# Kernel optimization log

Measured on AMD Instinct MI355X. Metric: run time of the kernel, lower is better.

The kernel has to match this reference:

```python
import jax, jax.numpy as jnp
import numpy as np

M_BUCKETS = 2048  # input_features // q = 4096 // 2


def countsketch(x, hash_idx, rand_sgn, m=M_BUCKETS):
    # x: [N, D]; scatter-add signed columns into m buckets -> [N, m]
    return jnp.zeros((x.shape[0], m), x.dtype).at[:, hash_idx].add(x * rand_sgn[None, :])


def setup_inputs() -> dict:
    key = jax.random.key(0)
    k1, k2, k3, k4, k5 = jax.random.split(key, 5)
    B, D, O = 4096, 4096, 4096
    inp = jax.random.normal(k1, (B, D), dtype=jnp.float32)
    # match torch init: weight uniform(-sqrt(3)/sqrt(D), sqrt(3)/sqrt(D)), bias uniform(-1/sqrt(D), 1/sqrt(D))
    bound = 1.0 / np.sqrt(D)
    weight = jax.random.uniform(k2, (O, D), dtype=jnp.float32,
                                minval=-bound * np.sqrt(3.0), maxval=bound * np.sqrt(3.0))
    bias = jax.random.uniform(k3, (O,), dtype=jnp.float32, minval=-bound, maxval=bound)
    hash_idx = jax.random.randint(k4, (D,), 0, M_BUCKETS, dtype=jnp.int32)
    rand_sgn = (2.0 * jax.random.randint(k5, (D,), 0, 2).astype(jnp.float32) - 1.0)
    return {"input": inp, "weight": weight, "bias": bias,
            "hash_idx": hash_idx, "rand_sgn": rand_sgn}


def reference(input, weight, bias, hash_idx, rand_sgn):
    input_sketch = countsketch(input, hash_idx, rand_sgn)    # [B, m]
    weight_sketch = countsketch(weight, hash_idx, rand_sgn)  # [O, m]
    out = input_sketch @ weight_sketch.T + bias[None, :]     # [B, O]
    return out
```

## Files before the change

kernel.cpp:

```cpp
#include <hip/hip_runtime.h>
#include <hip/hip_bf16.h>
#include <stdint.h>

#define D_DIM     4096
#define MB        2048
#define NROWS     4096
#define K_DIM     MB

typedef __bf16 bf16x8 __attribute__((ext_vector_type(8)));
typedef float  floatx4 __attribute__((ext_vector_type(4)));

__device__ __forceinline__ void gld_lds16(const void* g, void* l) {
    __builtin_amdgcn_global_load_lds(
        (const __attribute__((address_space(1))) unsigned int*)g,
        (__attribute__((address_space(3))) unsigned int*)l,
        16, 0, 0);
}

__global__ __launch_bounds__(256) void build_csr(
    const int* __restrict__ hash_idx,
    unsigned int* __restrict__ desc,
    unsigned short* __restrict__ perm16)
{
    __shared__ int cnt[MB];
    __shared__ int scan[MB];
    const int t = threadIdx.x;

    for (int k = t; k < MB; k += 256) cnt[k] = 0;
    __syncthreads();
    for (int j = t; j < D_DIM; j += 256) atomicAdd(&cnt[hash_idx[j]], 1);
    __syncthreads();
    for (int k = t; k < MB; k += 256) scan[k] = cnt[k];
    __syncthreads();
    for (int stride = 1; stride < MB; stride <<= 1) {
        int vals[8];
        #pragma unroll
        for (int i = 0; i < 8; ++i) {
            int k = t + 256 * i;
            vals[i] = (k >= stride) ? scan[k - stride] : 0;
        }
        __syncthreads();
        #pragma unroll
        for (int i = 0; i < 8; ++i) scan[t + 256 * i] += vals[i];
        __syncthreads();
    }
    for (int k = t; k < MB; k += 256) {
        int excl = scan[k] - cnt[k];
        desc[k] = ((unsigned)excl << 16) | (unsigned)cnt[k];
        cnt[k] = excl;
    }
    __syncthreads();
    for (int j = t; j < D_DIM; j += 256) {
        int k = hash_idx[j];
        int pos = atomicAdd(&cnt[k], 1);
        perm16[pos] = (unsigned short)j;
    }
}

__global__ __launch_bounds__(256) void sketch_gather(
    const float* __restrict__ input,
    const float* __restrict__ weight,
    const float* __restrict__ rand_sgn,
    const unsigned int* __restrict__ desc,
    const unsigned short* __restrict__ perm16,
    __hip_bfloat16* __restrict__ sk_in,
    __hip_bfloat16* __restrict__ sk_w)
{
    __shared__ __align__(16) float rv0[D_DIM + 8];
    __shared__ __align__(16) float rv1[D_DIM + 8];
    __shared__ __align__(16) unsigned short perm[D_DIM];
    const int b = blockIdx.x;
    const bool is_w = (b >= NROWS / 2);
    const int pr = is_w ? (b - NROWS / 2) : b;
    const float* src = (is_w ? weight : input) + (size_t)pr * 2 * D_DIM;
    __hip_bfloat16* dst = (is_w ? sk_w : sk_in) + (size_t)pr * 2 * MB;
    const int t = threadIdx.x;

    const uint4* pg = (const uint4*)perm16;
    ((uint4*)perm)[t]       = pg[t];
    ((uint4*)perm)[t + 256] = pg[t + 256];

    const float4* s4 = (const float4*)src;
    const float4* g4 = (const float4*)rand_sgn;
    #pragma unroll
    for (int i = 0; i < 4; ++i) {
        int q = t + 256 * i;
        float4 g = g4[q];
        float4 x0 = s4[q], x1 = s4[q + 1024];
        float4 y0; y0.x = x0.x*g.x; y0.y = x0.y*g.y; y0.z = x0.z*g.z; y0.w = x0.w*g.w;
        float4 y1; y1.x = x1.x*g.x; y1.y = x1.y*g.y; y1.z = x1.z*g.z; y1.w = x1.w*g.w;
        *(float4*)&rv0[4 * q] = y0;
        *(float4*)&rv1[4 * q] = y1;
    }
    __syncthreads();

    float4 a0[4], a1[4];
    #pragma unroll
    for (int i = 0; i < 4; ++i) {
        int q = t + 256 * i;
        ushort4 pp = *(const ushort4*)&perm[4 * q];
        a0[i].x = rv0[pp.x]; a0[i].y = rv0[pp.y];
        a0[i].z = rv0[pp.z]; a0[i].w = rv0[pp.w];
        a1[i].x = rv1[pp.x]; a1[i].y = rv1[pp.y];
        a1[i].z = rv1[pp.z]; a1[i].w = rv1[pp.w];
    }
    __syncthreads();
    #pragma unroll
    for (int i = 0; i < 4; ++i) {
        int q = t + 256 * i;
        *(float4*)&rv0[4 * q] = a0[i];
        *(float4*)&rv1[4 * q] = a1[i];
    }
    __syncthreads();

    #pragma unroll
    for (int i = 0; i < 8; ++i) {
        int k = t + 256 * i;
        unsigned d = desc[k];
        int st = (int)(d >> 16), c = (int)(d & 0xFFFF);
        float s0 = 0.f, s1 = 0.f;
        #pragma unroll
        for (int j = 0; j < 8; ++j) {
            float v0 = rv0[st + j], v1 = rv1[st + j];
            bool m = (j < c);
            s0 += m ? v0 : 0.f;
            s1 += m ? v1 : 0.f;
        }
        for (int j = 8; j < c; ++j) {
            s0 += rv0[st + j]; s1 += rv1[st + j];
        }
        dst[k]      = __float2bfloat16(s0);
        dst[MB + k] = __float2bfloat16(s1);
    }
}

__global__ __launch_bounds__(256) void gemm_bt_bias(
    const __hip_bfloat16* __restrict__ A,
    const __hip_bfloat16* __restrict__ B,
    const float* __restrict__ bias,
    float* __restrict__ C)
{
    __shared__ __align__(16) __hip_bfloat16 lA[128 * 64];
    __shared__ __align__(16) __hip_bfloat16 lB[128 * 64];

    const int t = threadIdx.x;
    const int lane = t & 63;
    const int wid  = t >> 6;
    const int warpM = wid & 1, warpN = wid >> 1;
    const int quad = lane >> 4;
    const int mrow = lane & 15;
    const int rowBase = blockIdx.y * 128;
    const int colBase = blockIdx.x * 128;

    const __hip_bfloat16* gA[4];
    const __hip_bfloat16* gB[4];
    #pragma unroll
    for (int p = 0; p < 4; ++p) {
        int G = t + 256 * p;
        int m = G >> 3;
        int q = (G & 7) ^ (m & 7);
        gA[p] = A + (size_t)(rowBase + m) * K_DIM + q * 8;
        gB[p] = B + (size_t)(colBase + m) * K_DIM + q * 8;
    }
    __hip_bfloat16* sA = &lA[t * 8];
    __hip_bfloat16* sB = &lB[t * 8];

    floatx4 acc[4][4];
    const floatx4 zero = {0.f, 0.f, 0.f, 0.f};
    #pragma unroll
    for (int i = 0; i < 4; ++i)
        #pragma unroll
        for (int j = 0; j < 4; ++j) acc[i][j] = zero;

    for (int kb = 0; kb < K_DIM; kb += 64) {
        #pragma unroll
        for (int p = 0; p < 4; ++p) {
            gld_lds16(gA[p] + kb, sA + p * 2048);
            gld_lds16(gB[p] + kb, sB + p * 2048);
        }
        __syncthreads();

        #pragma unroll
        for (int h = 0; h < 2; ++h) {
            bf16x8 af[4], bfr[4];
            #pragma unroll
            for (int i = 0; i < 4; ++i) {
                int mA = warpM * 64 + i * 16 + mrow;
                int sa = (h * 4 + quad) ^ (mA & 7);
                af[i] = *(const bf16x8*)&lA[(mA * 8 + sa) * 8];
                int mB = warpN * 64 + i * 16 + mrow;
                int sb = (h * 4 + quad) ^ (mB & 7);
                bfr[i] = *(const bf16x8*)&lB[(mB * 8 + sb) * 8];
            }
            #pragma unroll
            for (int i = 0; i < 4; ++i)
                #pragma unroll
                for (int j = 0; j < 4; ++j)
                    acc[i][j] = __builtin_amdgcn_mfma_f32_16x16x32_bf16(
                        af[i], bfr[j], acc[i][j], 0, 0, 0);
        }
        __syncthreads();
    }

    float bj[4];
    #pragma unroll
    for (int j = 0; j < 4; ++j) bj[j] = bias[colBase + warpN * 64 + j * 16 + mrow];
    #pragma unroll
    for (int i = 0; i < 4; ++i) {
        int m0 = rowBase + warpM * 64 + i * 16 + quad * 4;
        #pragma unroll
        for (int j = 0; j < 4; ++j) {
            int n = colBase + warpN * 64 + j * 16 + mrow;
            #pragma unroll
            for (int p = 0; p < 4; ++p)
                C[(size_t)(m0 + p) * NROWS + n] = acc[i][j][p] + bj[j];
        }
    }
}

extern "C" void kernel_launch(void* const* d_in, const int* in_sizes, int n_in,
                              void* d_out, int out_size, void* d_ws, size_t ws_size,
                              hipStream_t stream) {
    const float* input  = (const float*)d_in[0];
    const float* weight = (const float*)d_in[1];
    const float* bias   = (const float*)d_in[2];
    const int*   hidx   = (const int*)d_in[3];
    const float* sgn    = (const float*)d_in[4];
    float* out = (float*)d_out;

    char* ws = (char*)d_ws;
    __hip_bfloat16* sk_in = (__hip_bfloat16*)ws;
    __hip_bfloat16* sk_w  = (__hip_bfloat16*)(ws + (size_t)16 * 1024 * 1024);
    unsigned int*   desc  = (unsigned int*)(ws + (size_t)32 * 1024 * 1024);
    unsigned short* perm16 = (unsigned short*)(ws + (size_t)32 * 1024 * 1024 + 8192);

    build_csr<<<1, 256, 0, stream>>>(hidx, desc, perm16);
    sketch_gather<<<NROWS, 256, 0, stream>>>(input, weight, sgn, desc, perm16,
                                             sk_in, sk_w);
    gemm_bt_bias<<<dim3(32, 32), 256, 0, stream>>>(sk_in, sk_w, bias, out);
}
```

Measured before the change: 261.9 us.

## Rewrite sketch GEMM as 256x256-tile, 8-wave, double-buffered pipelined MFMA kernel

The bf16 GEMM moves from 128x128 tiles with 4 waves and one LDS buffer to 256x256 tiles with 8 waves and a 128 KB double-buffered LDS. Global-to-LDS loads for the next K tile are spread across eight sub-phases and interleaved with MFMA quadrants, using explicit barriers, vmcnt waits and setprio. The aim is to hide load latency behind MFMA work and raise data reuse per tile. In exchange, register pressure and LDS use per block go up, and the hand-written schedule and XOR swizzle are fragile.

```diff
diff --git a/kernel.cpp b/kernel.cpp
--- a/kernel.cpp
+++ b/kernel.cpp
@@ -134,83 +134,138 @@
     }
 }
 
-__global__ __launch_bounds__(256) void gemm_bt_bias(
+#define LDSA(p, h) (lds + (p)*32768 + (h)*16384)
+#define LDSB(p, h) (lds + 65536 + (p)*32768 + (h)*16384)
+
+#define BAR() do { __builtin_amdgcn_sched_barrier(0); \
+                   __builtin_amdgcn_s_barrier(); \
+                   __builtin_amdgcn_sched_barrier(0); } while (0)
+#define VMCNT4() asm volatile("s_waitcnt vmcnt(4)" ::: "memory")
+
+#define STAGE_A(p, mh, kt) do { \
+    int L_ = (mh)*8192 + t*16; \
+    int P_ = L_ ^ ((L_ & 512) >> 4); \
+    const char* s_ = Ab + (size_t)(rowBase + (P_ >> 7)) * 4096 \
+                        + (size_t)((((kt) & 31) * 128) + (P_ & 127)); \
+    gld_lds16(s_,                       LDSA(p, 0) + L_); \
+    gld_lds16(s_ + (size_t)128 * 4096,  LDSA(p, 1) + L_); \
+} while (0)
+
+#define STAGE_B(p, nh, kt) do { \
+    int L_ = (t >> 8) * 8192 + (nh)*4096 + (t & 255) * 16; \
+    int P_ = L_ ^ ((L_ & 512) >> 4); \
+    const char* s_ = Bb + (size_t)(colBase + (P_ >> 7)) * 4096 \
+                        + (size_t)((((kt) & 31) * 128) + (P_ & 127)); \
+    gld_lds16(s_,                       LDSB(p, 0) + L_); \
+    gld_lds16(s_ + (size_t)128 * 4096,  LDSB(p, 1) + L_); \
+} while (0)
+
+#define LOAD_A(p, mh) do { \
+    const char* ba_ = LDSA(p, wm); \
+    _Pragma("unroll") \
+    for (int i_ = 0; i_ < 4; ++i_) { \
+        int r_ = (mh)*64 + i_*16 + mrow; \
+        _Pragma("unroll") \
+        for (int kk_ = 0; kk_ < 2; ++kk_) { \
+            int L_ = r_*128 + kk_*64 + quad*16; \
+            af[i_][kk_] = *(const bf16x8*)(ba_ + (L_ ^ ((L_ & 512) >> 4))); \
+        } \
+    } \
+} while (0)
+
+#define LOAD_B(p, nh) do { \
+    const char* bb_ = LDSB(p, wn >> 1); \
+    _Pragma("unroll") \
+    for (int j_ = 0; j_ < 2; ++j_) { \
+        int r_ = (wn & 1)*64 + (nh)*32 + j_*16 + mrow; \
+        _Pragma("unroll") \
+        for (int kk_ = 0; kk_ < 2; ++kk_) { \
+            int L_ = r_*128 + kk_*64 + quad*16; \
+            bfrag[j_][kk_] = *(const bf16x8*)(bb_ + (L_ ^ ((L_ & 512) >> 4))); \
+        } \
+    } \
+} while (0)
+
+#define MFMA_Q(mh, nh) do { \
+    __builtin_amdgcn_s_setprio(1); \
+    _Pragma("unroll") \
+    for (int i_ = 0; i_ < 4; ++i_) \
+        _Pragma("unroll") \
+        for (int j_ = 0; j_ < 2; ++j_) \
+            _Pragma("unroll") \
+            for (int kk_ = 0; kk_ < 2; ++kk_) \
+                acc[(mh)*4 + i_][(nh)*2 + j_] = \
+                    __builtin_amdgcn_mfma_f32_16x16x32_bf16( \
+                        af[i_][kk_], bfrag[j_][kk_], \
+                        acc[(mh)*4 + i_][(nh)*2 + j_], 0, 0, 0); \
+    __builtin_amdgcn_s_setprio(0); \
+} while (0)
+
+__global__ __launch_bounds__(512, 2) void gemm_bt_bias(
     const __hip_bfloat16* __restrict__ A,
     const __hip_bfloat16* __restrict__ B,
     const float* __restrict__ bias,
     float* __restrict__ C)
 {
-    __shared__ __align__(16) __hip_bfloat16 lA[128 * 64];
-    __shared__ __align__(16) __hip_bfloat16 lB[128 * 64];
+    __shared__ __align__(16) char lds[131072];
+    const char* Ab = (const char*)A;
+    const char* Bb = (const char*)B;
 
     const int t = threadIdx.x;
     const int lane = t & 63;
     const int wid  = t >> 6;
-    const int warpM = wid & 1, warpN = wid >> 1;
+    const int wm = wid >> 2;
+    const int wn = wid & 3;
     const int quad = lane >> 4;
     const int mrow = lane & 15;
-    const int rowBase = blockIdx.y * 128;
-    const int colBase = blockIdx.x * 128;
-
-    const __hip_bfloat16* gA[4];
-    const __hip_bfloat16* gB[4];
-    #pragma unroll
-    for (int p = 0; p < 4; ++p) {
-        int G = t + 256 * p;
-        int m = G >> 3;
-        int q = (G & 7) ^ (m & 7);
-        gA[p] = A + (size_t)(rowBase + m) * K_DIM + q * 8;
-        gB[p] = B + (size_t)(colBase + m) * K_DIM + q * 8;
-    }
-    __hip_bfloat16* sA = &lA[t * 8];
-    __hip_bfloat16* sB = &lB[t * 8];
-
-    floatx4 acc[4][4];
+    const int rowBase = blockIdx.y * 256;
+    const int colBase = blockIdx.x * 256;
+
+    bf16x8 af[4][2];
+    bf16x8 bfrag[2][2];
+    floatx4 acc[8][4];
     const floatx4 zero = {0.f, 0.f, 0.f, 0.f};
     #pragma unroll
-    for (int i = 0; i < 4; ++i)
+    for (int i = 0; i < 8; ++i)
         #pragma unroll
         for (int j = 0; j < 4; ++j) acc[i][j] = zero;
 
-    for (int kb = 0; kb < K_DIM; kb += 64) {
-        #pragma unroll
-        for (int p = 0; p < 4; ++p) {
-            gld_lds16(gA[p] + kb, sA + p * 2048);
-            gld_lds16(gB[p] + kb, sB + p * 2048);
-        }
-        __syncthreads();
-
-        #pragma unroll
-        for (int h = 0; h < 2; ++h) {
-            bf16x8 af[4], bfr[4];
-            #pragma unroll
-            for (int i = 0; i < 4; ++i) {
-                int mA = warpM * 64 + i * 16 + mrow;
-                int sa = (h * 4 + quad) ^ (mA & 7);
-                af[i] = *(const bf16x8*)&lA[(mA * 8 + sa) * 8];
-                int mB = warpN * 64 + i * 16 + mrow;
-                int sb = (h * 4 + quad) ^ (mB & 7);
-                bfr[i] = *(const bf16x8*)&lB[(mB * 8 + sb) * 8];
-            }
-            #pragma unroll
-            for (int i = 0; i < 4; ++i)
-                #pragma unroll
-                for (int j = 0; j < 4; ++j)
-                    acc[i][j] = __builtin_amdgcn_mfma_f32_16x16x32_bf16(
-                        af[i], bfr[j], acc[i][j], 0, 0, 0);
-        }
-        __syncthreads();
+    STAGE_A(0, 0, 0); STAGE_B(0, 1, 0); STAGE_B(0, 0, 0); STAGE_A(0, 1, 0);
+    STAGE_A(1, 0, 1); STAGE_B(1, 1, 1);
+    VMCNT4();
+    BAR();
+
+    #pragma unroll 1
+    for (int it = 0; it < 16; ++it) {
+        const int kt = 2 * it;
+        LOAD_A(0, 0); LOAD_B(0, 0); STAGE_B(1, 0, kt + 1);
+        BAR(); MFMA_Q(0, 0); BAR();
+        LOAD_B(0, 1); STAGE_A(1, 1, kt + 1);
+        BAR(); MFMA_Q(0, 1); BAR();
+        LOAD_A(0, 1); STAGE_A(0, 0, kt + 2);
+        BAR(); MFMA_Q(1, 1); BAR();
+        LOAD_B(0, 0); STAGE_B(0, 1, kt + 2);
+        BAR(); MFMA_Q(1, 0); VMCNT4(); BAR();
+        LOAD_A(1, 0); LOAD_B(1, 0); STAGE_B(0, 0, kt + 2);
+        BAR(); MFMA_Q(0, 0); BAR();
+        LOAD_B(1, 1); STAGE_A(0, 1, kt + 2);
+        BAR(); MFMA_Q(0, 1); BAR();
+        LOAD_A(1, 1); STAGE_A(1, 0, kt + 3);
+        BAR(); MFMA_Q(1, 1); BAR();
+        LOAD_B(1, 0); STAGE_B(1, 1, kt + 3);
+        BAR(); MFMA_Q(1, 0); VMCNT4(); BAR();
     }
 
     float bj[4];
     #pragma unroll
-    for (int j = 0; j < 4; ++j) bj[j] = bias[colBase + warpN * 64 + j * 16 + mrow];
-    #pragma unroll
-    for (int i = 0; i < 4; ++i) {
-        int m0 = rowBase + warpM * 64 + i * 16 + quad * 4;
+    for (int j = 0; j < 4; ++j)
+        bj[j] = bias[colBase + wn * 64 + j * 16 + mrow];
+    #pragma unroll
+    for (int i = 0; i < 8; ++i) {
+        int m0 = rowBase + wm * 128 + i * 16 + quad * 4;
         #pragma unroll
         for (int j = 0; j < 4; ++j) {
-            int n = colBase + warpN * 64 + j * 16 + mrow;
+            int n = colBase + wn * 64 + j * 16 + mrow;
             #pragma unroll
             for (int p = 0; p < 4; ++p)
                 C[(size_t)(m0 + p) * NROWS + n] = acc[i][j][p] + bj[j];
@@ -237,5 +292,5 @@
     build_csr<<<1, 256, 0, stream>>>(hidx, desc, perm16);
     sketch_gather<<<NROWS, 256, 0, stream>>>(input, weight, sgn, desc, perm16,
                                              sk_in, sk_w);
-    gemm_bt_bias<<<dim3(32, 32), 256, 0, stream>>>(sk_in, sk_w, bias, out);
-}
+    gemm_bt_bias<<<dim3(16, 16), 512, 0, stream>>>(sk_in, sk_w, bias, out);
+}
```

After: 262.1 us. About the same (+0.1%).
